# Kernel tuning notes

Hardware: AMD Instinct MI355X
Metric: run time of the kernel (lower is better)

## Reference

```python
import jax, jax.numpy as jnp
import numpy as np

B = 1024
IN_DIM = 165
COND = 150
EMB = 150
MB_OUT = 10
MB_INT = 50
FEAT = IN_DIM + EMB  # 315

def _w(key, shape, fan_in):
    return jax.random.normal(key, shape, dtype=jnp.float32) / np.float32(np.sqrt(fan_in))

def setup_inputs() -> dict:
    key = jax.random.key(0)
    ks = jax.random.split(key, 10)
    return {
        "time_series": jax.random.normal(ks[0], (B, IN_DIM), dtype=jnp.float32),
        "condition": jax.random.randint(ks[1], (B,), 0, COND, dtype=jnp.int64) if jax.config.jax_enable_x64 else jax.random.randint(ks[1], (B,), 0, COND, dtype=jnp.int32),
        "emb": jax.random.normal(ks[2], (COND, EMB), dtype=jnp.float32),
        "T": jax.random.normal(ks[3], (FEAT, MB_OUT, MB_INT), dtype=jnp.float32),
        "W1": _w(ks[4], (FEAT + MB_OUT, 1536), FEAT + MB_OUT),
        "b1": jnp.zeros((1536,), jnp.float32),
        "W2": _w(ks[5], (1536, 1024), 1536),
        "b2": jnp.zeros((1024,), jnp.float32),
        "W3": _w(ks[6], (1024, 512), 1024),
        "b3": jnp.zeros((512,), jnp.float32),
        "W4": _w(ks[7], (512, 256), 512),
        "b4": jnp.zeros((256,), jnp.float32),
        "W5": _w(ks[8], (256, 1), 256),
        "b5": jnp.zeros((1,), jnp.float32),
    }

def reference(time_series, condition, emb, T, W1, b1, W2, b2, W3, b3, W4, b4, W5, b5):
    # embedding lookup + concat -> x: [B, 315]
    y = emb[condition]
    x = jnp.concatenate([time_series, y], axis=1)
    # minibatch discrimination: M: [B, out, inter]
    M = jnp.einsum('bf,fok->bok', x, T)
    # pairwise L1 over intermediate dim -> [B, B, out]
    abs_diff = jnp.sum(jnp.abs(M[:, None, :, :] - M[None, :, :, :]), axis=3)
    mb_feats = jnp.exp(-abs_diff).sum(axis=1)  # [B, out] (includes self term exp(0)=1)
    h = jnp.concatenate([x, mb_feats], axis=1)  # [B, 325]
    lrelu = lambda v: jax.nn.leaky_relu(v, 0.2)
    h = lrelu(h @ W1 + b1)  # dropout is identity in eval mode
    h = lrelu(h @ W2 + b2)
    h = lrelu(h @ W3 + b3)
    h = lrelu(h @ W4 + b4)
    return jax.nn.sigmoid(h @ W5 + b5)  # [B, 1]
```

## Files before the change

kernel.cpp:

```cpp
#include <hip/hip_runtime.h>
#include <hip/hip_bf16.h>

#define B_N     1024
#define IN_DIM  165
#define EMB_D   150
#define FEAT    315
#define H0_W    325
#define H0_S    352
#define MB_OUT  10
#define MB_INT  50
#define MROW    64
#define NPROJ   12

typedef __attribute__((ext_vector_type(8))) short short8;
typedef __attribute__((ext_vector_type(4))) float f32x4;

__device__ __forceinline__ ushort f2bf(float f) {
    uint u = __float_as_uint(f);
    return (ushort)((u + 0x7fffu + ((u >> 16) & 1u)) >> 16);
}
__device__ __forceinline__ uint pack_split(float v) {
    ushort h = f2bf(v);
    float hf = __uint_as_float((uint)h << 16);
    ushort l = f2bf(v - hf);
    return (uint)h | ((uint)l << 16);
}
__device__ __forceinline__ float unpack_split(uint u) {
    return __uint_as_float(u << 16) + __uint_as_float(u & 0xffff0000u);
}

__global__ __launch_bounds__(320) void build_x_kernel(
    const float* __restrict__ ts, const int* __restrict__ cond,
    const float* __restrict__ emb, uint* __restrict__ h0p)
{
    int b = blockIdx.x, t = threadIdx.x;
    if (t < 37) h0p[b * H0_S + FEAT + t] = 0u;
    float v;
    if (t < IN_DIM)      v = ts[b * IN_DIM + t];
    else if (t < FEAT)   v = emb[cond[b] * EMB_D + (t - IN_DIM)];
    else return;
    h0p[b * H0_S + t] = pack_split(v);
}

__global__ __launch_bounds__(256) void prep_kernel(
    const float* __restrict__ ts, const int* __restrict__ cond,
    const float* __restrict__ emb, const float* __restrict__ T,
    const float* __restrict__ W1, const float* __restrict__ W2,
    const float* __restrict__ W3, const float* __restrict__ W4,
    uint* __restrict__ h0p, uint* __restrict__ Tp, uint* __restrict__ Wb)
{
    int i = blockIdx.x * 256 + threadIdx.x;
    if (i < 163840) {
        int k = i >> 9, n = i & 511;
        float v = (k < FEAT && n < 500) ? T[k * 500 + n] : 0.f;
        Tp[i] = pack_split(v);
    } else if (i < 1548288) {
        int j = i - 163840;
        float v0 = 0.f, v1 = 0.f;
        if (j < 270336) {
            int k = j / 768, n = (j - k * 768) * 2;
            if (k < H0_W) { v0 = W1[k * 1536 + n]; v1 = W1[k * 1536 + n + 1]; }
        } else if (j < 1056768) {
            int jj = j - 270336;
            int k = jj >> 9, n = (jj & 511) * 2;
            v0 = W2[k * 1024 + n]; v1 = W2[k * 1024 + n + 1];
        } else if (j < 1318912) {
            int jj = j - 1056768;
            int k = jj >> 8, n = (jj & 255) * 2;
            v0 = W3[k * 512 + n]; v1 = W3[k * 512 + n + 1];
        } else {
            int jj = j - 1318912;
            int k = jj >> 7, n = (jj & 127) * 2;
            v0 = W4[k * 256 + n]; v1 = W4[k * 256 + n + 1];
        }
        Wb[j] = (uint)f2bf(v0) | ((uint)f2bf(v1) << 16);
    } else if (i < 1908736) {
        int j = i - 1548288;
        int b = j / H0_S, c = j - b * H0_S;
        uint o = 0u;
        if (c < IN_DIM)    o = pack_split(ts[b * IN_DIM + c]);
        else if (c < FEAT) o = pack_split(emb[cond[b] * EMB_D + (c - IN_DIM)]);
        h0p[b * H0_S + c] = o;
    }
}

template<int EPI, int PACKED>
__global__ __launch_bounds__(256) void gemm_mfma(
    const uint*  __restrict__ Ap, const void* __restrict__ Bw,
    const float* __restrict__ bias, void* __restrict__ Cout,
    int N, int K, int lda, int ldb, int ldc,
    int kIterTotal, int Ks, float* __restrict__ Pout)
{
    __shared__ ushort Ah[64 * 32], Al[64 * 32], Bh[64 * 32], Bl[64 * 32];

    const int t    = threadIdx.x;
    const int bm   = blockIdx.y << 6;
    const int bn   = blockIdx.x << 6;
    const int wid  = t >> 6, lane = t & 63;
    const int wm   = (wid >> 1) << 5, wn = (wid & 1) << 5;
    const int lm   = lane & 15, lc = lane >> 4;

    const int ar  = t >> 2, ac = t & 3;
    const int bn2 = t & 63, bk = t >> 6;

    const int z   = blockIdx.z;
    const int it0 = z * Ks;
    const int nIt = min(Ks, kIterTotal - it0);

    const int aw = ar  * 32 + ((ac ^ (ar  & 3)) << 3);
    const int bw = bn2 * 32 + ((bk ^ (bn2 & 3)) << 3);
    const int sw = (lc ^ (lm & 3)) << 3;
    const int a0 = (wm + lm)      * 32 + sw;
    const int a1 = (wm + 16 + lm) * 32 + sw;
    const int b0 = (wn + lm)      * 32 + sw;
    const int b1 = (wn + 16 + lm) * 32 + sw;

    uint curA[8], nxtA[8], curB[8], nxtB[8];

    auto loadA = [&](int k0, uint* dst) {
        const uint* p = Ap + (bm + ar) * lda + k0 + (ac << 3);
        uint4 v0 = *(const uint4*)p;
        uint4 v1 = *(const uint4*)(p + 4);
        dst[0] = v0.x; dst[1] = v0.y; dst[2] = v0.z; dst[3] = v0.w;
        dst[4] = v1.x; dst[5] = v1.y; dst[6] = v1.z; dst[7] = v1.w;
    };
    auto loadB = [&](int k0, uint* dst) {
        int kb = k0 + (bk << 3);
        if (PACKED) {
            const uint* p = (const uint*)Bw + kb * ldb + bn + bn2;
            #pragma unroll
            for (int j = 0; j < 8; ++j) dst[j] = p[j * ldb];
        } else {
            const float* p = (const float*)Bw + kb * ldb + bn + bn2;
            bool cok = (bn + bn2) < N;
            #pragma unroll
            for (int j = 0; j < 8; ++j)
                dst[j] = __float_as_uint((cok && (kb + j) < K) ? p[j * ldb] : 0.f);
        }
    };

    f32x4 acc[2][2] = {};

    loadA(it0 << 5, curA);
    loadB(it0 << 5, curB);

    for (int it = 0; it < nIt; ++it) {
        short8 vah, val, vbh, vbl;
        #pragma unroll
        for (int j = 0; j < 8; ++j) {
            uint ua = curA[j];
            vah[j] = (short)(ua & 0xffffu);
            val[j] = (short)(ua >> 16);
            if (PACKED) {
                uint ub = curB[j];
                vbh[j] = (short)(ub & 0xffffu);
                vbl[j] = (short)(ub >> 16);
            } else {
                float v = __uint_as_float(curB[j]);
                ushort h = f2bf(v);
                float hf = __uint_as_float((uint)h << 16);
                vbh[j] = (short)h;
                vbl[j] = (short)f2bf(v - hf);
            }
        }
        __syncthreads();
        *(short8*)&Ah[aw] = vah;
        *(short8*)&Al[aw] = val;
        *(short8*)&Bh[bw] = vbh;
        *(short8*)&Bl[bw] = vbl;
        __syncthreads();

        if (it + 1 < nIt) {
            loadA((it0 + it + 1) << 5, nxtA);
            loadB((it0 + it + 1) << 5, nxtB);
        }

        short8 fah0 = *(const short8*)&Ah[a0];
        short8 fah1 = *(const short8*)&Ah[a1];
        short8 fal0 = *(const short8*)&Al[a0];
        short8 fal1 = *(const short8*)&Al[a1];
        short8 fbh0 = *(const short8*)&Bh[b0];
        short8 fbh1 = *(const short8*)&Bh[b1];
        short8 fbl0 = *(const short8*)&Bl[b0];
        short8 fbl1 = *(const short8*)&Bl[b1];

        acc[0][0] = __builtin_amdgcn_mfma_f32_16x16x32_bf16(fah0, fbh0, acc[0][0], 0, 0, 0);
        acc[0][1] = __builtin_amdgcn_mfma_f32_16x16x32_bf16(fah0, fbh1, acc[0][1], 0, 0, 0);
        acc[1][0] = __builtin_amdgcn_mfma_f32_16x16x32_bf16(fah1, fbh0, acc[1][0], 0, 0, 0);
        acc[1][1] = __builtin_amdgcn_mfma_f32_16x16x32_bf16(fah1, fbh1, acc[1][1], 0, 0, 0);
        acc[0][0] = __builtin_amdgcn_mfma_f32_16x16x32_bf16(fah0, fbl0, acc[0][0], 0, 0, 0);
        acc[0][1] = __builtin_amdgcn_mfma_f32_16x16x32_bf16(fah0, fbl1, acc[0][1], 0, 0, 0);
        acc[1][0] = __builtin_amdgcn_mfma_f32_16x16x32_bf16(fah1, fbl0, acc[1][0], 0, 0, 0);
        acc[1][1] = __builtin_amdgcn_mfma_f32_16x16x32_bf16(fah1, fbl1, acc[1][1], 0, 0, 0);
        acc[0][0] = __builtin_amdgcn_mfma_f32_16x16x32_bf16(fal0, fbh0, acc[0][0], 0, 0, 0);
        acc[0][1] = __builtin_amdgcn_mfma_f32_16x16x32_bf16(fal0, fbh1, acc[0][1], 0, 0, 0);
        acc[1][0] = __builtin_amdgcn_mfma_f32_16x16x32_bf16(fal1, fbh0, acc[1][0], 0, 0, 0);
        acc[1][1] = __builtin_amdgcn_mfma_f32_16x16x32_bf16(fal1, fbh1, acc[1][1], 0, 0, 0);

        #pragma unroll
        for (int j = 0; j < 8; ++j) { curA[j] = nxtA[j]; curB[j] = nxtB[j]; }
    }

    if (gridDim.z > 1) {
        float* P = Pout + (size_t)z * B_N * N;
        #pragma unroll
        for (int mi = 0; mi < 2; ++mi)
        #pragma unroll
        for (int ni = 0; ni < 2; ++ni)
        #pragma unroll
        for (int r = 0; r < 4; ++r) {
            int row = bm + wm + mi * 16 + lc * 4 + r;
            int col = bn + wn + ni * 16 + lm;
            if (col < N) P[row * N + col] = acc[mi][ni][r];
        }
        return;
    }

    #pragma unroll
    for (int mi = 0; mi < 2; ++mi)
    #pragma unroll
    for (int ni = 0; ni < 2; ++ni)
    #pragma unroll
    for (int r = 0; r < 4; ++r) {
        int row = bm + wm + mi * 16 + lc * 4 + r;
        int col = bn + wn + ni * 16 + lm;
        float v = acc[mi][ni][r];
        if (EPI == 0) {
            v += bias[col];
            v = (v > 0.f) ? v : 0.2f * v;
            ((uint*)Cout)[row * ldc + col] = pack_split(v);
        } else {
            if (col < N) {
                int o = col / MB_INT, kk = col - o * MB_INT;
                ((float*)Cout)[(o * B_N + row) * MROW + kk] = v;
            }
        }
    }
}

__global__ __launch_bounds__(256) void gemm_mfma2(
    const uint* __restrict__ Ap, const ushort* __restrict__ Bw,
    const float* __restrict__ bias, uint* __restrict__ Cout,
    int N, int lda, int ldb, int ldc,
    int kIterTotal, int Ks, float* __restrict__ Pout)
{
    __shared__ ushort Ah[64 * 32], Al[64 * 32], Bh[64 * 32];

    const int t    = threadIdx.x;
    const int bm   = blockIdx.y << 6;
    const int bn   = blockIdx.x << 6;
    const int wid  = t >> 6, lane = t & 63;
    const int wm   = (wid >> 1) << 5, wn = (wid & 1) << 5;
    const int lm   = lane & 15, lc = lane >> 4;

    const int ar  = t >> 2, ac = t & 3;
    const int bn2 = t & 63, bk = t >> 6;

    const int z   = blockIdx.z;
    const int it0 = z * Ks;
    const int nIt = min(Ks, kIterTotal - it0);

    const int aw = ar  * 32 + ((ac ^ (ar  & 3)) << 3);
    const int bw = bn2 * 32 + ((bk ^ (bn2 & 3)) << 3);
    const int sw = (lc ^ (lm & 3)) << 3;
    const int a0 = (wm + lm)      * 32 + sw;
    const int a1 = (wm + 16 + lm) * 32 + sw;
    const int b0 = (wn + lm)      * 32 + sw;
    const int b1 = (wn + 16 + lm) * 32 + sw;

    uint   curA[8], nxtA[8];
    ushort curB[8], nxtB[8];

    auto loadA = [&](int k0, uint* dst) {
        const uint* p = Ap + (bm + ar) * lda + k0 + (ac << 3);
        uint4 v0 = *(const uint4*)p;
        uint4 v1 = *(const uint4*)(p + 4);
        dst[0] = v0.x; dst[1] = v0.y; dst[2] = v0.z; dst[3] = v0.w;
        dst[4] = v1.x; dst[5] = v1.y; dst[6] = v1.z; dst[7] = v1.w;
    };
    auto loadB = [&](int k0, ushort* dst) {
        const ushort* p = Bw + (k0 + (bk << 3)) * ldb + bn + bn2;
        #pragma unroll
        for (int j = 0; j < 8; ++j) dst[j] = p[j * ldb];
    };

    f32x4 acc[2][2] = {};

    loadA(it0 << 5, curA);
    loadB(it0 << 5, curB);

    for (int it = 0; it < nIt; ++it) {
        short8 vah, val, vbh;
        #pragma unroll
        for (int j = 0; j < 8; ++j) {
            uint ua = curA[j];
            vah[j] = (short)(ua & 0xffffu);
            val[j] = (short)(ua >> 16);
            vbh[j] = (short)curB[j];
        }
        __syncthreads();
        *(short8*)&Ah[aw] = vah;
        *(short8*)&Al[aw] = val;
        *(short8*)&Bh[bw] = vbh;
        __syncthreads();

        if (it + 1 < nIt) {
            loadA((it0 + it + 1) << 5, nxtA);
            loadB((it0 + it + 1) << 5, nxtB);
        }

        short8 fah0 = *(const short8*)&Ah[a0];
        short8 fah1 = *(const short8*)&Ah[a1];
        short8 fal0 = *(const short8*)&Al[a0];
        short8 fal1 = *(const short8*)&Al[a1];
        short8 fbh0 = *(const short8*)&Bh[b0];
        short8 fbh1 = *(const short8*)&Bh[b1];

        acc[0][0] = __builtin_amdgcn_mfma_f32_16x16x32_bf16(fah0, fbh0, acc[0][0], 0, 0, 0);
        acc[0][1] = __builtin_amdgcn_mfma_f32_16x16x32_bf16(fah0, fbh1, acc[0][1], 0, 0, 0);
        acc[1][0] = __builtin_amdgcn_mfma_f32_16x16x32_bf16(fah1, fbh0, acc[1][0], 0, 0, 0);
        acc[1][1] = __builtin_amdgcn_mfma_f32_16x16x32_bf16(fah1, fbh1, acc[1][1], 0, 0, 0);
        acc[0][0] = __builtin_amdgcn_mfma_f32_16x16x32_bf16(fal0, fbh0, acc[0][0], 0, 0, 0);
        acc[0][1] = __builtin_amdgcn_mfma_f32_16x16x32_bf16(fal0, fbh1, acc[0][1], 0, 0, 0);
        acc[1][0] = __builtin_amdgcn_mfma_f32_16x16x32_bf16(fal1, fbh0, acc[1][0], 0, 0, 0);
        acc[1][1] = __builtin_amdgcn_mfma_f32_16x16x32_bf16(fal1, fbh1, acc[1][1], 0, 0, 0);

        #pragma unroll
        for (int j = 0; j < 8; ++j) { curA[j] = nxtA[j]; curB[j] = nxtB[j]; }
    }

    if (gridDim.z > 1) {
        float* P = Pout + (size_t)z * B_N * N;
        #pragma unroll
        for (int mi = 0; mi < 2; ++mi)
        #pragma unroll
        for (int ni = 0; ni < 2; ++ni)
        #pragma unroll
        for (int r = 0; r < 4; ++r) {
            int row = bm + wm + mi * 16 + lc * 4 + r;
            int col = bn + wn + ni * 16 + lm;
            P[row * N + col] = acc[mi][ni][r];
        }
        return;
    }

    #pragma unroll
    for (int mi = 0; mi < 2; ++mi)
    #pragma unroll
    for (int ni = 0; ni < 2; ++ni)
    #pragma unroll
    for (int r = 0; r < 4; ++r) {
        int row = bm + wm + mi * 16 + lc * 4 + r;
        int col = bn + wn + ni * 16 + lm;
        float v = acc[mi][ni][r] + bias[col];
        v = (v > 0.f) ? v : 0.2f * v;
        Cout[row * ldc + col] = pack_split(v);
    }
}

template<int FINAL>
__global__ __launch_bounds__(256) void epi_pack_kernel(
    const float* __restrict__ P, const float* __restrict__ bias,
    uint* __restrict__ outp, int n4, int S,
    const float* __restrict__ W5, const float* __restrict__ b5,
    float* __restrict__ out)
{
    const int c4 = blockIdx.x * 64 + (threadIdx.x & 63);
    const int r  = blockIdx.y * 4 + (threadIdx.x >> 6);
    const int idx = r * n4 + c4;
    const float4* P4 = (const float4*)P;
    float4 v = P4[idx];
    for (int s = 1; s < S; ++s) {
        float4 w = P4[(size_t)s * B_N * n4 + idx];
        v.x += w.x; v.y += w.y; v.z += w.z; v.w += w.w;
    }
    float4 bb = ((const float4*)bias)[c4];
    v.x += bb.x; v.y += bb.y; v.z += bb.z; v.w += bb.w;
    v.x = (v.x > 0.f) ? v.x : 0.2f * v.x;
    v.y = (v.y > 0.f) ? v.y : 0.2f * v.y;
    v.z = (v.z > 0.f) ? v.z : 0.2f * v.z;
    v.w = (v.w > 0.f) ? v.w : 0.2f * v.w;
    if (FINAL) {
        const float4 w5 = ((const float4*)W5)[c4];
        float s = v.x * w5.x + v.y * w5.y + v.z * w5.z + v.w * w5.w;
        #pragma unroll
        for (int off = 32; off > 0; off >>= 1)
            s += __shfl_xor(s, off);
        if ((threadIdx.x & 63) == 0) {
            float z = s + b5[0];
            out[r] = 1.f / (1.f + __expf(-z));
        }
    } else {
        uint4 o;
        o.x = pack_split(v.x); o.y = pack_split(v.y);
        o.z = pack_split(v.z); o.w = pack_split(v.w);
        ((uint4*)outp)[idx] = o;
    }
}

__global__ __launch_bounds__(256) void epi_m2_kernel(
    const float* __restrict__ P, float* __restrict__ M2, int S)
{
    int i = blockIdx.x * 256 + threadIdx.x;
    if (i >= B_N * 500) return;
    int r = i / 500, c = i - r * 500;
    float v = P[i];
    for (int s = 1; s < S; ++s) v += P[(size_t)s * B_N * 500 + i];
    int o = c / MB_INT, k = c - o * MB_INT;
    M2[(o * B_N + r) * MROW + k] = v;
}

__device__ __constant__ const unsigned long long PMASK[NPROJ] = {
    0x2B5F1E3A4B6C7DULL, 0x19D4A7C3E85B26ULL, 0x3E6A1D59F0B483ULL,
    0x07C2F8A135E9D6ULL, 0x2A94E6B7D01C3FULL, 0x35B8D2041A7E6CULL,
    0x1CE07B3F68A5D2ULL, 0x22F1A4C85D93E0ULL, 0x0B67D3E92C50F8ULL,
    0x38A0C5171E4B9DULL, 0x114E92F6A3D078ULL, 0x2D73B0E84F169AULL
};

template<int J0>
__device__ __forceinline__ void proj3(const float* __restrict__ row, float* s) {
    float s0 = 0.f, s1 = 0.f, s2 = 0.f;
    #pragma unroll
    for (int k = 0; k < MB_INT; ++k) {
        float v = row[k];
        if ((PMASK[J0]     >> k) & 1ULL) s0 -= v; else s0 += v;
        if ((PMASK[J0 + 4] >> k) & 1ULL) s1 -= v; else s1 += v;
        if ((PMASK[J0 + 8] >> k) & 1ULL) s2 -= v; else s2 += v;
    }
    s[0] = s0; s[1] = s1; s[2] = s2;
}

__global__ __launch_bounds__(256) void proj_kernel(
    const float* __restrict__ M2, float* __restrict__ Rproj)
{
    __shared__ float Ls[64 * 53];
    const int rt = blockIdx.x, o = blockIdx.y, t = threadIdx.x;

    #pragma unroll
    for (int i = 0; i < 13; ++i) {
        int idx = t + i * 256;
        int r = idx / 52, k = idx - r * 52;
        float v = (k < MB_INT) ? M2[(o * B_N + rt * 64 + r) * MROW + k] : 0.f;
        Ls[r * 53 + k] = v;
    }
    __syncthreads();

    const int r = t & 63, j0 = t >> 6;
    float s[3];
    if      (j0 == 0) proj3<0>(&Ls[r * 53], s);
    else if (j0 == 1) proj3<1>(&Ls[r * 53], s);
    else if (j0 == 2) proj3<2>(&Ls[r * 53], s);
    else              proj3<3>(&Ls[r * 53], s);

    float* dst = Rproj + (size_t)(o * B_N + rt * 64 + r) * NPROJ;
    dst[j0] = s[0]; dst[j0 + 4] = s[1]; dst[j0 + 8] = s[2];
}

__global__ __launch_bounds__(256) void pairwise_kernel(
    const float* __restrict__ M2, const float* __restrict__ Rproj,
    float* __restrict__ part)
{
    __shared__ float Lp[32 * NPROJ];
    const int grp = blockIdx.x, o = blockIdx.y, ch = blockIdx.z;
    const int t = threadIdx.x, wid = t >> 6, lane = t & 63;

    if (t < 96)
        ((float4*)Lp)[t] = ((const float4*)(Rproj + (size_t)(o * B_N + ch * 32) * NPROJ))[t];
    __syncthreads();

    const int b = (grp * 4 + wid) * 64 + lane;

    const float4* Ar = (const float4*)(M2 + (size_t)(o * B_N + b) * MROW);
    float4 A0 = Ar[0], A1 = Ar[1], A2 = Ar[2],  A3 = Ar[3];
    float4 A4 = Ar[4], A5 = Ar[5], A6 = Ar[6],  A7 = Ar[7];
    float4 A8 = Ar[8], A9 = Ar[9], A10 = Ar[10], A11 = Ar[11];
    float2 A12 = *(const float2*)((const float*)Ar + 48);

    const float4* Pr = (const float4*)(Rproj + (size_t)(o * B_N + b) * NPROJ);
    float4 P0 = Pr[0], P1 = Pr[1], P2 = Pr[2];

    const int selfstep = (ch == (b >> 5)) ? (b & 31) : -1;
    float acc = (selfstep >= 0) ? 1.f : 0.f;

    const float* Bbase = M2 + (size_t)(o * B_N + ch * 32) * MROW;

    for (int b2 = 0; b2 < 32; ++b2) {
        const float4* qp = (const float4*)&Lp[b2 * NPROJ];
        float4 q0 = qp[0], q1 = qp[1], q2 = qp[2];
        float d0 = fabsf(P0.x - q0.x), d1 = fabsf(P0.y - q0.y);
        float d2 = fabsf(P0.z - q0.z), d3 = fabsf(P0.w - q0.w);
        float d4 = fabsf(P1.x - q1.x), d5 = fabsf(P1.y - q1.y);
        float d6 = fabsf(P1.z - q1.z), d7 = fabsf(P1.w - q1.w);
        float d8 = fabsf(P2.x - q2.x), d9 = fabsf(P2.y - q2.y);
        float dA = fabsf(P2.z - q2.z), dB = fabsf(P2.w - q2.w);
        float m0 = fmaxf(fmaxf(d0, d1), fmaxf(d2, d3));
        float m1 = fmaxf(fmaxf(d4, d5), fmaxf(d6, d7));
        float m2 = fmaxf(fmaxf(d8, d9), fmaxf(dA, dB));
        float dmax = fmaxf(fmaxf(m0, m1), m2);

        if (__all(dmax > 110.f || b2 == selfstep)) continue;

        const float4* q = (const float4*)(Bbase + b2 * MROW);
        float4 s = {0.f, 0.f, 0.f, 0.f};
        float4 v;
        v = q[0];  s.x += fabsf(A0.x - v.x);  s.y += fabsf(A0.y - v.y);  s.z += fabsf(A0.z - v.z);  s.w += fabsf(A0.w - v.w);
        v = q[1];  s.x += fabsf(A1.x - v.x);  s.y += fabsf(A1.y - v.y);  s.z += fabsf(A1.z - v.z);  s.w += fabsf(A1.w - v.w);
        v = q[2];  s.x += fabsf(A2.x - v.x);  s.y += fabsf(A2.y - v.y);  s.z += fabsf(A2.z - v.z);  s.w += fabsf(A2.w - v.w);
        v = q[3];  s.x += fabsf(A3.x - v.x);  s.y += fabsf(A3.y - v.y);  s.z += fabsf(A3.z - v.z);  s.w += fabsf(A3.w - v.w);
        v = q[4];  s.x += fabsf(A4.x - v.x);  s.y += fabsf(A4.y - v.y);  s.z += fabsf(A4.z - v.z);  s.w += fabsf(A4.w - v.w);
        v = q[5];  s.x += fabsf(A5.x - v.x);  s.y += fabsf(A5.y - v.y);  s.z += fabsf(A5.z - v.z);  s.w += fabsf(A5.w - v.w);
        v = q[6];  s.x += fabsf(A6.x - v.x);  s.y += fabsf(A6.y - v.y);  s.z += fabsf(A6.z - v.z);  s.w += fabsf(A6.w - v.w);
        v = q[7];  s.x += fabsf(A7.x - v.x);  s.y += fabsf(A7.y - v.y);  s.z += fabsf(A7.z - v.z);  s.w += fabsf(A7.w - v.w);
        v = q[8];  s.x += fabsf(A8.x - v.x);  s.y += fabsf(A8.y - v.y);  s.z += fabsf(A8.z - v.z);  s.w += fabsf(A8.w - v.w);
        v = q[9];  s.x += fabsf(A9.x - v.x);  s.y += fabsf(A9.y - v.y);  s.z += fabsf(A9.z - v.z);  s.w += fabsf(A9.w - v.w);
        v = q[10]; s.x += fabsf(A10.x - v.x); s.y += fabsf(A10.y - v.y); s.z += fabsf(A10.z - v.z); s.w += fabsf(A10.w - v.w);
        v = q[11]; s.x += fabsf(A11.x - v.x); s.y += fabsf(A11.y - v.y); s.z += fabsf(A11.z - v.z); s.w += fabsf(A11.w - v.w);
        v = q[12]; s.x += fabsf(A12.x - v.x); s.y += fabsf(A12.y - v.y);
        float d = (s.x + s.y) + (s.z + s.w);
        float e = __expf(-d);
        acc += (b2 == selfstep) ? 0.f : e;
    }
    part[(ch * MB_OUT + o) * B_N + b] = acc;
}

__global__ __launch_bounds__(256) void mb_reduce_kernel(
    const float* __restrict__ part, uint* __restrict__ h0p)
{
    int i = blockIdx.x * 256 + threadIdx.x;
    if (i < MB_OUT * B_N) {
        int o = i / B_N, b = i - o * B_N;
        float s = 0.f;
        #pragma unroll
        for (int ch = 0; ch < 32; ++ch)
            s += part[(ch * MB_OUT + o) * B_N + b];
        h0p[b * H0_S + FEAT + o] = pack_split(s);
    }
}

__global__ __launch_bounds__(256) void final_kernel(
    const uint* __restrict__ h4p, const float* __restrict__ W5,
    const float* __restrict__ b5, float* __restrict__ out)
{
    const int wave = threadIdx.x >> 6;
    const int lane = threadIdx.x & 63;
    const int row  = blockIdx.x * 4 + wave;

    const uint4  h = ((const uint4*)(h4p + row * 256))[lane];
    const float4 w = ((const float4*)W5)[lane];
    float s = unpack_split(h.x) * w.x + unpack_split(h.y) * w.y
            + unpack_split(h.z) * w.z + unpack_split(h.w) * w.w;
    #pragma unroll
    for (int off = 32; off > 0; off >>= 1)
        s += __shfl_xor(s, off);
    if (lane == 0) {
        float z = s + b5[0];
        out[row] = 1.f / (1.f + __expf(-z));
    }
}

extern "C" void kernel_launch(void* const* d_in, const int* in_sizes, int n_in,
                              void* d_out, int out_size, void* d_ws, size_t ws_size,
                              hipStream_t stream)
{
    const float* ts   = (const float*)d_in[0];
    const int*   cond = (const int*)  d_in[1];
    const float* emb  = (const float*)d_in[2];
    const float* T    = (const float*)d_in[3];
    const float* W1   = (const float*)d_in[4];
    const float* b1   = (const float*)d_in[5];
    const float* W2   = (const float*)d_in[6];
    const float* b2   = (const float*)d_in[7];
    const float* W3   = (const float*)d_in[8];
    const float* b3   = (const float*)d_in[9];
    const float* W4   = (const float*)d_in[10];
    const float* b4   = (const float*)d_in[11];
    const float* W5   = (const float*)d_in[12];
    const float* b5   = (const float*)d_in[13];
    float* out = (float*)d_out;

    uint*  h0p  = (uint*)d_ws;
    float* M2   = (float*)(h0p + 360448);
    uint*  h1p  = (uint*)(M2 + 655360);
    uint*  h2p  = h1p + 1572864;
    uint*  h3p  = (uint*)M2;
    uint*  h4p  = h1p;
    float* part  = (float*)h1p;
    float* Rproj = part + 327680;
    const size_t baseU = 360448 + 655360 + 1572864 + 1048576;

    uint* Tp = (uint*)d_ws + baseU;
    uint* Wb = Tp + 163840;
    ushort* W1b = (ushort*)Wb;
    ushort* W2b = W1b + 540672;
    ushort* W3b = W2b + 1572864;
    ushort* W4b = W3b + 524288;
    const size_t packU = 163840 + 1384448;
    const bool packed = (ws_size / 4) >= (baseU + packU);

    const size_t pbase = packed ? baseU + packU : baseU;
    size_t capU = (ws_size / 4 > pbase) ? ws_size / 4 - pbase : 0;
    float* Pbuf = (float*)((uint*)d_ws + pbase);

    auto fits = [&](int s, int N) { return (size_t)s * B_N * N <= capU; };
    const int ST = fits(2, 500)  ? 2 : 1;
    const int S1 = fits(3, 1536) ? 3 : (fits(2, 1536) ? 2 : 1);
    const int S2 = fits(3, 1024) ? 3 : (fits(2, 1024) ? 2 : 1);
    const int S3 = fits(4, 512)  ? 4 : (fits(2, 512)  ? 2 : 1);
    const int S4 = fits(4, 256)  ? 4 : (fits(2, 256)  ? 2 : 1);

    if (packed) {
        prep_kernel<<<7456, 256, 0, stream>>>(ts, cond, emb, T, W1, W2, W3, W4,
                                              h0p, Tp, Wb);

        {
            int kit = 10, ks = (kit + ST - 1) / ST;
            dim3 g(8, 16, ST);
            gemm_mfma<1,1><<<g, 256, 0, stream>>>(h0p, Tp, nullptr, M2,
                                                  500, FEAT, H0_S, 512, 0, kit, ks, Pbuf);
            if (ST > 1)
                epi_m2_kernel<<<(B_N * 500 + 255) / 256, 256, 0, stream>>>(Pbuf, M2, ST);
        }

        { dim3 g(16, MB_OUT); proj_kernel<<<g, 256, 0, stream>>>(M2, Rproj); }
        { dim3 g(4, MB_OUT, 32); pairwise_kernel<<<g, 256, 0, stream>>>(M2, Rproj, part); }
        mb_reduce_kernel<<<(MB_OUT * B_N + 255) / 256, 256, 0, stream>>>(part, h0p);

        auto runL2 = [&](const uint* in, const ushort* Wbp, const float* bia,
                         uint* outp, int N, int lda, int kit, int S, bool fin) {
            int ks = (kit + S - 1) / S;
            dim3 g(N / 64, 16, S);
            gemm_mfma2<<<g, 256, 0, stream>>>(in, Wbp, bia, outp, N, lda, N, N,
                                              kit, ks, Pbuf);
            if (S > 1) {
                dim3 ge((N / 4) / 64, B_N / 4);
                if (fin)
                    epi_pack_kernel<1><<<ge, 256, 0, stream>>>(Pbuf, bia, outp, N / 4, S,
                                                               W5, b5, out);
                else
                    epi_pack_kernel<0><<<ge, 256, 0, stream>>>(Pbuf, bia, outp, N / 4, S,
                                                               nullptr, nullptr, nullptr);
            }
        };

        runL2(h0p, W1b, b1, h1p, 1536, H0_S, 11, S1, false);
        runL2(h1p, W2b, b2, h2p, 1024, 1536, 48, S2, false);
        runL2(h2p, W3b, b3, h3p,  512, 1024, 32, S3, false);
        runL2(h3p, W4b, b4, h4p,  256,  512, 16, S4, true);
        if (S4 <= 1)
            final_kernel<<<B_N / 4, 256, 0, stream>>>(h4p, W5, b5, out);
    } else {
        build_x_kernel<<<B_N, 320, 0, stream>>>(ts, cond, emb, h0p);
        { dim3 g(8, 16); gemm_mfma<1,0><<<g, 256, 0, stream>>>(
              h0p, T, nullptr, M2, 500, FEAT, H0_S, 500, 0, 10, 10, Pbuf); }
        { dim3 g(16, MB_OUT); proj_kernel<<<g, 256, 0, stream>>>(M2, Rproj); }
        { dim3 g(4, MB_OUT, 32); pairwise_kernel<<<g, 256, 0, stream>>>(M2, Rproj, part); }
        mb_reduce_kernel<<<(MB_OUT * B_N + 255) / 256, 256, 0, stream>>>(part, h0p);
        { dim3 g(24, 16); gemm_mfma<0,0><<<g, 256, 0, stream>>>(
              h0p, W1, b1, h1p, 1536, H0_W, H0_S, 1536, 1536, 11, 11, Pbuf); }
        { dim3 g(16, 16); gemm_mfma<0,0><<<g, 256, 0, stream>>>(
              h1p, W2, b2, h2p, 1024, 1536, 1536, 1024, 1024, 48, 48, Pbuf); }
        { dim3 g(8, 16);  gemm_mfma<0,0><<<g, 256, 0, stream>>>(
              h2p, W3, b3, h3p, 512, 1024, 1024, 512, 512, 32, 32, Pbuf); }
        { dim3 g(4, 16);  gemm_mfma<0,0><<<g, 256, 0, stream>>>(
              h3p, W4, b4, h4p, 256, 512, 512, 256, 256, 16, 16, Pbuf); }
        final_kernel<<<B_N / 4, 256, 0, stream>>>(h4p, W5, b5, out);
    }
}
```

Baseline: 102.7 us.

## Store hidden activations as single bf16 and fuse M2 split-K reduction into projection

Hidden activations h1..h4 are now stored as plain bf16 instead of a hi/lo split pair. Layers 2-4 use a new single-pass MFMA GEMM that issues one bf16 MFMA per tile pair instead of the split-precision path, which halves activation traffic and cuts MFMA work. Separately, the split-K reduction for the minibatch projection M is folded into proj_kernel, which removes one kernel launch and one round trip through memory. The cost is lower activation precision for the MLP layers, which may loosen accuracy against the fp32 reference.

```diff
diff --git a/kernel.cpp b/kernel.cpp
--- a/kernel.cpp
+++ b/kernel.cpp
@@ -27,6 +27,9 @@
 }
 __device__ __forceinline__ float unpack_split(uint u) {
     return __uint_as_float(u << 16) + __uint_as_float(u & 0xffff0000u);
+}
+__device__ __forceinline__ float bf2f(ushort u) {
+    return __uint_as_float((uint)u << 16);
 }
 
 __global__ __launch_bounds__(320) void build_x_kernel(
@@ -240,7 +243,7 @@
 
 __global__ __launch_bounds__(256) void gemm_mfma2(
     const uint* __restrict__ Ap, const ushort* __restrict__ Bw,
-    const float* __restrict__ bias, uint* __restrict__ Cout,
+    const float* __restrict__ bias, ushort* __restrict__ Cout,
     int N, int lda, int ldb, int ldc,
     int kIterTotal, int Ks, float* __restrict__ Pout)
 {
@@ -354,14 +357,120 @@
         int col = bn + wn + ni * 16 + lm;
         float v = acc[mi][ni][r] + bias[col];
         v = (v > 0.f) ? v : 0.2f * v;
-        Cout[row * ldc + col] = pack_split(v);
+        Cout[row * ldc + col] = f2bf(v);
+    }
+}
+
+__global__ __launch_bounds__(256) void gemm_mfma1(
+    const ushort* __restrict__ Ab, const ushort* __restrict__ Bw,
+    const float* __restrict__ bias, ushort* __restrict__ Cout,
+    int N, int lda, int ldb, int ldc,
+    int kIterTotal, int Ks, float* __restrict__ Pout)
+{
+    __shared__ ushort Ah[64 * 32], Bh[64 * 32];
+
+    const int t    = threadIdx.x;
+    const int bm   = blockIdx.y << 6;
+    const int bn   = blockIdx.x << 6;
+    const int wid  = t >> 6, lane = t & 63;
+    const int wm   = (wid >> 1) << 5, wn = (wid & 1) << 5;
+    const int lm   = lane & 15, lc = lane >> 4;
+
+    const int ar  = t >> 2, ac = t & 3;
+    const int bn2 = t & 63, bk = t >> 6;
+
+    const int z   = blockIdx.z;
+    const int it0 = z * Ks;
+    const int nIt = min(Ks, kIterTotal - it0);
+
+    const int aw = ar  * 32 + ((ac ^ (ar  & 3)) << 3);
+    const int bw = bn2 * 32 + ((bk ^ (bn2 & 3)) << 3);
+    const int sw = (lc ^ (lm & 3)) << 3;
+    const int a0 = (wm + lm)      * 32 + sw;
+    const int a1 = (wm + 16 + lm) * 32 + sw;
+    const int b0 = (wn + lm)      * 32 + sw;
+    const int b1 = (wn + 16 + lm) * 32 + sw;
+
+    short8 curA, nxtA;
+    ushort curB[8], nxtB[8];
+
+    auto loadA = [&](int k0, short8* dst) {
+        const ushort* p = Ab + (size_t)(bm + ar) * lda + k0 + (ac << 3);
+        *dst = *(const short8*)p;
+    };
+    auto loadB = [&](int k0, ushort* dst) {
+        const ushort* p = Bw + (k0 + (bk << 3)) * ldb + bn + bn2;
+        #pragma unroll
+        for (int j = 0; j < 8; ++j) dst[j] = p[j * ldb];
+    };
+
+    f32x4 acc[2][2] = {};
+
+    loadA(it0 << 5, &curA);
+    loadB(it0 << 5, curB);
+
+    for (int it = 0; it < nIt; ++it) {
+        short8 vbh;
+        #pragma unroll
+        for (int j = 0; j < 8; ++j) vbh[j] = (short)curB[j];
+        __syncthreads();
+        *(short8*)&Ah[aw] = curA;
+        *(short8*)&Bh[bw] = vbh;
+        __syncthreads();
+
+        if (it + 1 < nIt) {
+            loadA((it0 + it + 1) << 5, &nxtA);
+            loadB((it0 + it + 1) << 5, nxtB);
+        }
+
+        short8 fa0 = *(const short8*)&Ah[a0];
+        short8 fa1 = *(const short8*)&Ah[a1];
+        short8 fb0 = *(const short8*)&Bh[b0];
+        short8 fb1 = *(const short8*)&Bh[b1];
+
+        acc[0][0] = __builtin_amdgcn_mfma_f32_16x16x32_bf16(fa0, fb0, acc[0][0], 0, 0, 0);
+        acc[0][1] = __builtin_amdgcn_mfma_f32_16x16x32_bf16(fa0, fb1, acc[0][1], 0, 0, 0);
+        acc[1][0] = __builtin_amdgcn_mfma_f32_16x16x32_bf16(fa1, fb0, acc[1][0], 0, 0, 0);
+        acc[1][1] = __builtin_amdgcn_mfma_f32_16x16x32_bf16(fa1, fb1, acc[1][1], 0, 0, 0);
+
+        curA = nxtA;
+        #pragma unroll
+        for (int j = 0; j < 8; ++j) curB[j] = nxtB[j];
+    }
+
+    if (gridDim.z > 1) {
+        float* P = Pout + (size_t)z * B_N * N;
+        #pragma unroll
+        for (int mi = 0; mi < 2; ++mi)
+        #pragma unroll
+        for (int ni = 0; ni < 2; ++ni)
+        #pragma unroll
+        for (int r = 0; r < 4; ++r) {
+            int row = bm + wm + mi * 16 + lc * 4 + r;
+            int col = bn + wn + ni * 16 + lm;
+            P[row * N + col] = acc[mi][ni][r];
+        }
+        return;
+    }
+
+    #pragma unroll
+    for (int mi = 0; mi < 2; ++mi)
+    #pragma unroll
+    for (int ni = 0; ni < 2; ++ni)
+    #pragma unroll
+    for (int r = 0; r < 4; ++r) {
+        int row = bm + wm + mi * 16 + lc * 4 + r;
+        int col = bn + wn + ni * 16 + lm;
+        float v = acc[mi][ni][r] + bias[col];
+        v = (v > 0.f) ? v : 0.2f * v;
+        Cout[row * ldc + col] = f2bf(v);
     }
 }
 
 template<int FINAL>
 __global__ __launch_bounds__(256) void epi_pack_kernel(
     const float* __restrict__ P, const float* __restrict__ bias,
-    uint* __restrict__ outp, int n4, int S,
+    ushort* __restrict__ outp, int n4, int S,
     const float* __restrict__ W5, const float* __restrict__ b5,
     float* __restrict__ out)
 {
@@ -391,23 +500,10 @@
             out[r] = 1.f / (1.f + __expf(-z));
         }
     } else {
-        uint4 o;
-        o.x = pack_split(v.x); o.y = pack_split(v.y);
-        o.z = pack_split(v.z); o.w = pack_split(v.w);
-        ((uint4*)outp)[idx] = o;
-    }
-}
-
-__global__ __launch_bounds__(256) void epi_m2_kernel(
-    const float* __restrict__ P, float* __restrict__ M2, int S)
-{
-    int i = blockIdx.x * 256 + threadIdx.x;
-    if (i >= B_N * 500) return;
-    int r = i / 500, c = i - r * 500;
-    float v = P[i];
-    for (int s = 1; s < S; ++s) v += P[(size_t)s * B_N * 500 + i];
-    int o = c / MB_INT, k = c - o * MB_INT;
-    M2[(o * B_N + r) * MROW + k] = v;
+        ushort4 o;
+        o.x = f2bf(v.x); o.y = f2bf(v.y); o.z = f2bf(v.z); o.w = f2bf(v.w);
+        ((ushort4*)outp)[idx] = o;
+    }
 }
 
 __device__ __constant__ const unsigned long long PMASK[NPROJ] = {
@@ -431,7 +527,8 @@
 }
 
 __global__ __launch_bounds__(256) void proj_kernel(
-    const float* __restrict__ M2, float* __restrict__ Rproj)
+    float* __restrict__ M2, float* __restrict__ Rproj,
+    const float* __restrict__ P, int ST)
 {
     __shared__ float Ls[64 * 53];
     const int rt = blockIdx.x, o = blockIdx.y, t = threadIdx.x;
@@ -440,7 +537,18 @@
     for (int i = 0; i < 13; ++i) {
         int idx = t + i * 256;
         int r = idx / 52, k = idx - r * 52;
-        float v = (k < MB_INT) ? M2[(o * B_N + rt * 64 + r) * MROW + k] : 0.f;
+        int row = rt * 64 + r;
+        float v = 0.f;
+        if (k < MB_INT) {
+            if (ST > 1) {
+                const float* q = P + (size_t)row * 500 + o * MB_INT + k;
+                v = q[0];
+                for (int s = 1; s < ST; ++s) v += q[(size_t)s * B_N * 500];
+                M2[(o * B_N + row) * MROW + k] = v;
+            } else {
+                v = M2[(o * B_N + row) * MROW + k];
+            }
+        }
         Ls[r * 53 + k] = v;
     }
     __syncthreads();
@@ -537,18 +645,27 @@
     }
 }
 
+template<int U16>
 __global__ __launch_bounds__(256) void final_kernel(
-    const uint* __restrict__ h4p, const float* __restrict__ W5,
+    const void* __restrict__ h4v, const float* __restrict__ W5,
     const float* __restrict__ b5, float* __restrict__ out)
 {
     const int wave = threadIdx.x >> 6;
     const int lane = threadIdx.x & 63;
     const int row  = blockIdx.x * 4 + wave;
 
-    const uint4  h = ((const uint4*)(h4p + row * 256))[lane];
     const float4 w = ((const float4*)W5)[lane];
-    float s = unpack_split(h.x) * w.x + unpack_split(h.y) * w.y
-            + unpack_split(h.z) * w.z + unpack_split(h.w) * w.w;
+    float s;
+    if (U16) {
+        const ushort* h4 = (const ushort*)h4v;
+        ushort4 h = ((const ushort4*)(h4 + (size_t)row * 256))[lane];
+        s = bf2f(h.x) * w.x + bf2f(h.y) * w.y + bf2f(h.z) * w.z + bf2f(h.w) * w.w;
+    } else {
+        const uint* h4 = (const uint*)h4v;
+        uint4 h = ((const uint4*)(h4 + (size_t)row * 256))[lane];
+        s = unpack_split(h.x) * w.x + unpack_split(h.y) * w.y
+          + unpack_split(h.z) * w.z + unpack_split(h.w) * w.w;
+    }
     #pragma unroll
     for (int off = 32; off > 0; off >>= 1)
         s += __shfl_xor(s, off);
@@ -617,19 +734,32 @@
             dim3 g(8, 16, ST);
             gemm_mfma<1,1><<<g, 256, 0, stream>>>(h0p, Tp, nullptr, M2,
                                                   500, FEAT, H0_S, 512, 0, kit, ks, Pbuf);
-            if (ST > 1)
-                epi_m2_kernel<<<(B_N * 500 + 255) / 256, 256, 0, stream>>>(Pbuf, M2, ST);
-        }
-
-        { dim3 g(16, MB_OUT); proj_kernel<<<g, 256, 0, stream>>>(M2, Rproj); }
+        }
+        { dim3 g(16, MB_OUT); proj_kernel<<<g, 256, 0, stream>>>(M2, Rproj, Pbuf, ST); }
         { dim3 g(4, MB_OUT, 32); pairwise_kernel<<<g, 256, 0, stream>>>(M2, Rproj, part); }
         mb_reduce_kernel<<<(MB_OUT * B_N + 255) / 256, 256, 0, stream>>>(part, h0p);
 
-        auto runL2 = [&](const uint* in, const ushort* Wbp, const float* bia,
-                         uint* outp, int N, int lda, int kit, int S, bool fin) {
+        ushort* h1u = (ushort*)h1p;
+        ushort* h2u = (ushort*)h2p;
+        ushort* h3u = (ushort*)h3p;
+        ushort* h4u = (ushort*)h4p;
+
+        {
+            int ks = (11 + S1 - 1) / S1;
+            dim3 g(24, 16, S1);
+            gemm_mfma2<<<g, 256, 0, stream>>>(h0p, W1b, b1, h1u, 1536, H0_S,
+                                              1536, 1536, 11, ks, Pbuf);
+            if (S1 > 1) {
+                dim3 ge(6, 256);
+                epi_pack_kernel<0><<<ge, 256, 0, stream>>>(Pbuf, b1, h1u, 384, S1,
+                                                           nullptr, nullptr, nullptr);
+            }
+        }
+        auto runL1 = [&](const ushort* in, const ushort* Wbp, const float* bia,
+                         ushort* outp, int N, int lda, int kit, int S, bool fin) {
             int ks = (kit + S - 1) / S;
             dim3 g(N / 64, 16, S);
-            gemm_mfma2<<<g, 256, 0, stream>>>(in, Wbp, bia, outp, N, lda, N, N,
+            gemm_mfma1<<<g, 256, 0, stream>>>(in, Wbp, bia, outp, N, lda, N, N,
                                               kit, ks, Pbuf);
             if (S > 1) {
                 dim3 ge((N / 4) / 64, B_N / 4);
@@ -641,18 +771,16 @@
                                                                nullptr, nullptr, nullptr);
             }
         };
-
-        runL2(h0p, W1b, b1, h1p, 1536, H0_S, 11, S1, false);
-        runL2(h1p, W2b, b2, h2p, 1024, 1536, 48, S2, false);
-        runL2(h2p, W3b, b3, h3p,  512, 1024, 32, S3, false);
-        runL2(h3p, W4b, b4, h4p,  256,  512, 16, S4, true);
+        runL1(h1u, W2b, b2, h2u, 1024, 1536, 48, S2, false);
+        runL1(h2u, W3b, b3, h3u,  512, 1024, 32, S3, false);
+        runL1(h3u, W4b, b4, h4u,  256,  512, 16, S4, true);
         if (S4 <= 1)
-            final_kernel<<<B_N / 4, 256, 0, stream>>>(h4p, W5, b5, out);
+            final_kernel<1><<<B_N / 4, 256, 0, stream>>>(h4u, W5, b5, out);
     } else {
         build_x_kernel<<<B_N, 320, 0, stream>>>(ts, cond, emb, h0p);
         { dim3 g(8, 16); gemm_mfma<1,0><<<g, 256, 0, stream>>>(
               h0p, T, nullptr, M2, 500, FEAT, H0_S, 500, 0, 10, 10, Pbuf); }
-        { dim3 g(16, MB_OUT); proj_kernel<<<g, 256, 0, stream>>>(M2, Rproj); }
+        { dim3 g(16, MB_OUT); proj_kernel<<<g, 256, 0, stream>>>(M2, Rproj, nullptr, 1); }
         { dim3 g(4, MB_OUT, 32); pairwise_kernel<<<g, 256, 0, stream>>>(M2, Rproj, part); }
         mb_reduce_kernel<<<(MB_OUT * B_N + 255) / 256, 256, 0, stream>>>(part, h0p);
         { dim3 g(24, 16); gemm_mfma<0,0><<<g, 256, 0, stream>>>(
@@ -663,6 +791,6 @@
               h2p, W3, b3, h3p, 512, 1024, 1024, 512, 512, 32, 32, Pbuf); }
         { dim3 g(4, 16);  gemm_mfma<0,0><<<g, 256, 0, stream>>>(
               h3p, W4, b4, h4p, 256, 512, 512, 256, 256, 16, 16, Pbuf); }
-        final_kernel<<<B_N / 4, 256, 0, stream>>>(h4p, W5, b5, out);
-    }
-}
+        final_kernel<0><<<B_N / 4, 256, 0, stream>>>(h4p, W5, b5, out);
+    }
+}
```

Result: faster. 97.92 us (-4.7%).
